# Performance work log

Hardware: AMD Instinct MI355X
Metric: run time of the kernel (lower is better)

Reference implementation:

```python
import jax, jax.numpy as jnp
import numpy as np

DIM = 1024
DIM_HEAD = 64
HEADS = 16
INNER = DIM_HEAD * HEADS
SCALE = 8.0
EPS_LN = 1e-5
EPS_L2 = 1e-12


def _layernorm(x, gamma):
    mu = jnp.mean(x, axis=-1, keepdims=True)
    var = jnp.var(x, axis=-1, keepdims=True)
    return (x - mu) / jnp.sqrt(var + EPS_LN) * gamma  # beta is a zero buffer


def _l2norm(t):
    n = jnp.linalg.norm(t, axis=-1, keepdims=True)
    return t / jnp.maximum(n, EPS_L2)


def setup_inputs() -> dict:
    key = jax.random.key(0)
    ks = jax.random.split(key, 8)
    b, n = 4, 2048
    x = jax.random.normal(ks[0], (b, n, DIM), dtype=jnp.float32)
    context_mask = jax.random.randint(ks[1], (b, n), 0, 2) > 0
    gamma = jnp.ones((DIM,), dtype=jnp.float32)
    wq = jax.random.normal(ks[2], (DIM, INNER), dtype=jnp.float32) * 0.02
    wkv = jax.random.normal(ks[3], (DIM, 2 * INNER), dtype=jnp.float32) * 0.02
    null_kv = jax.random.normal(ks[4], (2, HEADS, 1, DIM_HEAD), dtype=jnp.float32)
    q_scale = jnp.ones((DIM_HEAD,), dtype=jnp.float32)
    k_scale = jnp.ones((DIM_HEAD,), dtype=jnp.float32)
    wo = jax.random.normal(ks[5], (INNER, DIM), dtype=jnp.float32) * 0.02
    return {"x": x, "context_mask": context_mask, "gamma": gamma, "wq": wq,
            "wkv": wkv, "null_kv": null_kv, "q_scale": q_scale,
            "k_scale": k_scale, "wo": wo}


def reference(x, context_mask, gamma, wq, wkv, null_kv, q_scale, k_scale, wo):
    b, n, _ = x.shape
    xn = _layernorm(x, gamma)
    q = xn @ wq                     # [b, n, inner]
    kv = xn @ wkv                   # self-attention: kv_input = x
    k, v = jnp.split(kv, 2, axis=-1)

    def split_heads(t):
        return t.reshape(b, n, HEADS, DIM_HEAD).transpose(0, 2, 1, 3)  # b h n d

    q, k, v = map(split_heads, (q, k, v))
    nk = jnp.broadcast_to(null_kv[0][None], (b, HEADS, 1, DIM_HEAD))
    nv = jnp.broadcast_to(null_kv[1][None], (b, HEADS, 1, DIM_HEAD))
    k = jnp.concatenate([nk, k], axis=2)  # b h (n+1) d
    v = jnp.concatenate([nv, v], axis=2)

    q = _l2norm(q) * q_scale
    k = _l2norm(k) * k_scale

    sim = jnp.einsum('bhid,bhjd->bhij', q, k) * SCALE  # b h n (n+1)
    mask = jnp.pad(context_mask, ((0, 0), (1, 0)), constant_values=True)  # null kv always visible
    mask_value = -jnp.finfo(sim.dtype).max
    sim = jnp.where(mask[:, None, None, :], sim, mask_value)

    attn = jax.nn.softmax(sim, axis=-1)
    out = jnp.einsum('bhij,bhjd->bhid', attn, v)
    out = out.transpose(0, 2, 1, 3).reshape(b, n, INNER)
    return out @ wo
```

## Files before the change

kernel.cpp:

```cpp
#include <hip/hip_runtime.h>

typedef unsigned short u16;
typedef unsigned int u32;
typedef unsigned long long u64;
typedef __bf16 bf16x8 __attribute__((ext_vector_type(8)));
typedef float f32x4 __attribute__((ext_vector_type(4)));

#define B_ 4
#define N_ 2048
#define D_ 1024
#define H_ 16
#define DH_ 64
#define NKP_ 2112
#define NKT_ 33

__device__ __forceinline__ float bf2f(u16 u) {
  union { u32 i; float f; } v; v.i = ((u32)u) << 16; return v.f;
}
__device__ __forceinline__ u16 f2bf(float f) {
  union { float f; u32 i; } v; v.f = f;
  u32 r = v.i + 0x7fffu + ((v.i >> 16) & 1u);
  return (u16)(r >> 16);
}
__device__ __forceinline__ u32 cvtpk(float a, float b) {
  u32 r;
  asm("v_cvt_pk_bf16_f32 %0, %1, %2" : "=v"(r) : "v"(a), "v"(b));
  return r;
}
__device__ __forceinline__ void load_lds16(const void* g, void* l) {
  __builtin_amdgcn_global_load_lds((const __attribute__((address_space(1))) void*)g,
                                   (__attribute__((address_space(3))) void*)l, 16, 0, 0);
}

__global__ __launch_bounds__(256) void ln_kernel(const float* __restrict__ x,
                                                 const float* __restrict__ gamma,
                                                 u16* __restrict__ xn) {
  int row = blockIdx.x;
  int tid = threadIdx.x, lane = tid & 63, wid = tid >> 6;
  const float4 v = ((const float4*)(x + (size_t)row * D_))[tid];
  float s  = v.x + v.y + v.z + v.w;
  float ss = v.x * v.x + v.y * v.y + v.z * v.z + v.w * v.w;
#pragma unroll
  for (int off = 1; off < 64; off <<= 1) {
    s  += __shfl_xor(s,  off, 64);
    ss += __shfl_xor(ss, off, 64);
  }
  __shared__ float rs[4], rss[4];
  if (lane == 0) { rs[wid] = s; rss[wid] = ss; }
  __syncthreads();
  float S  = rs[0] + rs[1] + rs[2] + rs[3];
  float SS = rss[0] + rss[1] + rss[2] + rss[3];
  float mean = S * (1.0f / D_);
  float var  = SS * (1.0f / D_) - mean * mean;
  float inv  = rsqrtf(var + 1e-5f);
  const float4 g = ((const float4*)gamma)[tid];
  u16* o = xn + (size_t)row * D_ + tid * 4;
  o[0] = f2bf((v.x - mean) * inv * g.x);
  o[1] = f2bf((v.y - mean) * inv * g.y);
  o[2] = f2bf((v.z - mean) * inv * g.z);
  o[3] = f2bf((v.w - mean) * inv * g.w);
}

__global__ __launch_bounds__(256) void wt_kernel(const float* __restrict__ W,
                                                 u16* __restrict__ WT,
                                                 int K, int N) {
  __shared__ float t[32][33];
  int tiles_n = N >> 5;
  int tk = blockIdx.x / tiles_n, tn = blockIdx.x % tiles_n;
  int tx = threadIdx.x & 31, ty = threadIdx.x >> 5;
  int k0 = tk << 5, n0 = tn << 5;
#pragma unroll
  for (int i = 0; i < 4; ++i)
    t[ty + i * 8][tx] = W[(size_t)(k0 + ty + i * 8) * N + n0 + tx];
  __syncthreads();
#pragma unroll
  for (int i = 0; i < 4; ++i)
    WT[(size_t)(n0 + ty + i * 8) * K + k0 + tx] = f2bf(t[tx][ty + i * 8]);
}

__global__ __launch_bounds__(256) void prep_kernel(const int* __restrict__ mask,
                                                   const float* __restrict__ qs,
                                                   const float* __restrict__ ksc,
                                                   const float* __restrict__ null_kv,
                                                   u16* __restrict__ Kb,
                                                   u16* __restrict__ Vt,
                                                   float* __restrict__ cb) {
  __shared__ int cnts[4];
  int bh = blockIdx.x, h = bh & 15;
  int tid = threadIdx.x, lane = tid & 63, wid = tid >> 6;
  if (wid == 0) {
    float kv = null_kv[h * 64 + lane];
    float ss = kv * kv;
#pragma unroll
    for (int off = 1; off < 64; off <<= 1) ss += __shfl_xor(ss, off, 64);
    float inv = 1.0f / fmaxf(sqrtf(ss), 1e-12f);
    Kb[((size_t)bh * NKP_ + 2048) * 64 + lane] = f2bf(kv * inv * ksc[lane]);
    Vt[((size_t)bh * 64 + lane) * NKP_ + 2048] = f2bf(null_kv[1024 + h * 64 + lane]);
  }
  for (int i = tid; i < 63 * 64; i += 256) {
    int r = i >> 6, c = i & 63;
    Kb[((size_t)bh * NKP_ + 2049 + r) * 64 + c] = 0;
  }
  for (int i = tid; i < 64 * 63; i += 256) {
    int d = i / 63, c = i % 63;
    Vt[((size_t)bh * 64 + d) * NKP_ + 2049 + c] = 0;
  }
  if (bh == 0) {
    if (tid < 4) cnts[tid] = 0;
    __syncthreads();
    int c0 = 0, c1 = 0, c2 = 0, c3 = 0;
    for (int i = tid; i < B_ * N_; i += 256) {
      int z = (mask[i] == 0);
      int b = i >> 11;
      if (b == 0) c0 += z; else if (b == 1) c1 += z; else if (b == 2) c2 += z; else c3 += z;
    }
    atomicAdd(&cnts[0], c0); atomicAdd(&cnts[1], c1);
    atomicAdd(&cnts[2], c2); atomicAdd(&cnts[3], c3);
    __syncthreads();
    if (tid == 0) {
      float mw = 0.f;
      for (int i = 0; i < DH_; ++i) mw = fmaxf(mw, fabsf(qs[i] * ksc[i]));
      float cbias = -8.0f * mw * 1.4426950408889634f;
      cb[0] = cbias;
      float e = __builtin_amdgcn_exp2f(cbias);
#pragma unroll
      for (int b = 0; b < 4; ++b) cb[1 + b] = (float)(cnts[b] + 63) * e;
    }
  }
}

template <int MODE>
__global__ __launch_bounds__(256) void gemm_bt(const u16* __restrict__ A,
                                               const u16* __restrict__ Bt,
                                               void* __restrict__ Cv,
                                               int M, int N, int K,
                                               const float* __restrict__ qs,
                                               u16* __restrict__ Vt,
                                               const int* __restrict__ Mask) {
  __shared__ __attribute__((aligned(16))) u16 sm[2 * 128 * 64];
  u16* a_sm = sm;
  u16* b_sm = sm + 128 * 64;
  int tid = threadIdx.x, lane = tid & 63, wid = tid >> 6;
  int m0 = blockIdx.x * 128, n0 = blockIdx.y * 128;
  int wm = (wid >> 1) * 64, wn = (wid & 1) * 64;
  int sr = lane >> 3, sc = (lane & 7) * 8;
  int la = lane & 15, lk = (lane >> 4) * 8;
  f32x4 acc[4][4] = {};
  for (int k0 = 0; k0 < K; k0 += 64) {
    __syncthreads();
#pragma unroll
    for (int i = 0; i < 4; ++i) {
      int r = i * 32 + wid * 8;
      load_lds16(A  + (size_t)(m0 + r + sr) * K + k0 + sc, &a_sm[r * 64]);
      load_lds16(Bt + (size_t)(n0 + r + sr) * K + k0 + sc, &b_sm[r * 64]);
    }
    __syncthreads();
#pragma unroll
    for (int s = 0; s < 2; ++s) {
      bf16x8 af[4], bfr[4];
#pragma unroll
      for (int mf = 0; mf < 4; ++mf)
        af[mf] = *(const bf16x8*)&a_sm[(wm + mf * 16 + la) * 64 + s * 32 + lk];
#pragma unroll
      for (int nf = 0; nf < 4; ++nf)
        bfr[nf] = *(const bf16x8*)&b_sm[(wn + nf * 16 + la) * 64 + s * 32 + lk];
#pragma unroll
      for (int mf = 0; mf < 4; ++mf)
#pragma unroll
        for (int nf = 0; nf < 4; ++nf)
          acc[mf][nf] = __builtin_amdgcn_mfma_f32_16x16x32_bf16(af[mf], bfr[nf], acc[mf][nf], 0, 0, 0);
    }
  }
  int crow = (lane >> 4) * 4, ccol = lane & 15;

  if (MODE == 3) {
    int by = blockIdx.y;
    int rr0 = m0 + wm;
    int b = rr0 >> 11;
    int seq0 = rr0 & 2047;
    const int* mrow = Mask + b * N_ + seq0;
    if (by < 8) {
      int h = by * 2 + (wn >> 6);
      float kscv[4];
#pragma unroll
      for (int nf = 0; nf < 4; ++nf) kscv[nf] = qs[nf * 16 + ccol];
      u16* kb = (u16*)Cv + ((size_t)(b * 16 + h) * NKP_) * 64;
#pragma unroll
      for (int mf = 0; mf < 4; ++mf) {
        float invr[4]; int mvv[4];
#pragma unroll
        for (int r = 0; r < 4; ++r) {
          float ss = 0.f;
#pragma unroll
          for (int nf = 0; nf < 4; ++nf) ss += acc[mf][nf][r] * acc[mf][nf][r];
#pragma unroll
          for (int off = 1; off < 16; off <<= 1) ss += __shfl_xor(ss, off, 64);
          invr[r] = 1.0f / fmaxf(sqrtf(ss), 1e-12f);
          mvv[r] = mrow[mf * 16 + crow + r];
        }
#pragma unroll
        for (int nf = 0; nf < 4; ++nf)
#pragma unroll
          for (int r = 0; r < 4; ++r)
            kb[(size_t)(seq0 + mf * 16 + crow + r) * 64 + nf * 16 + ccol] =
                f2bf(mvv[r] ? acc[mf][nf][r] * invr[r] * kscv[nf] : 0.f);
      }
    } else {
      int h = (by - 8) * 2 + (wn >> 6);
      __syncthreads();
      u16* tw = sm + wid * 4096;
#pragma unroll
      for (int mf = 0; mf < 4; ++mf) {
        int mvv[4];
#pragma unroll
        for (int r = 0; r < 4; ++r) mvv[r] = mrow[mf * 16 + crow + r];
#pragma unroll
        for (int nf = 0; nf < 4; ++nf) {
          int row = nf * 16 + ccol;
#pragma unroll
          for (int r = 0; r < 4; ++r)
            tw[row * 64 + ((mf * 16 + crow + r) ^ ((row & 7) * 8))] =
                f2bf(mvv[r] ? acc[mf][nf][r] : 0.f);
        }
      }
      u16* vb = Vt + ((size_t)(b * 16 + h) * 64) * NKP_;
      int dr = lane >> 3, kc = (lane & 7) * 8;
#pragma unroll
      for (int i = 0; i < 8; ++i) {
        int d = i * 8 + dr;
        bf16x8 vv = *(const bf16x8*)&tw[d * 64 + (kc ^ ((d & 7) * 8))];
        *(bf16x8*)(vb + (size_t)d * NKP_ + seq0 + kc) = vv;
      }
    }
    return;
  }

  float qsv[4];
  if (MODE == 2) {
#pragma unroll
    for (int nf = 0; nf < 4; ++nf) qsv[nf] = qs[nf * 16 + ccol];
  }
#pragma unroll
  for (int mf = 0; mf < 4; ++mf) {
    float invr[4];
    if (MODE == 2) {
#pragma unroll
      for (int r = 0; r < 4; ++r) {
        float ss = 0.f;
#pragma unroll
        for (int nf = 0; nf < 4; ++nf) ss += acc[mf][nf][r] * acc[mf][nf][r];
#pragma unroll
        for (int off = 1; off < 16; off <<= 1) ss += __shfl_xor(ss, off, 64);
        invr[r] = 1.0f / fmaxf(sqrtf(ss), 1e-12f);
      }
    }
#pragma unroll
    for (int nf = 0; nf < 4; ++nf) {
      int rr = m0 + wm + mf * 16 + crow;
      int cc = n0 + wn + nf * 16 + ccol;
      if (MODE == 1) {
        float* C = (float*)Cv;
#pragma unroll
        for (int r = 0; r < 4; ++r) C[(size_t)(rr + r) * N + cc] = acc[mf][nf][r];
      } else if (MODE == 0) {
        u16* C = (u16*)Cv;
#pragma unroll
        for (int r = 0; r < 4; ++r) C[(size_t)(rr + r) * N + cc] = f2bf(acc[mf][nf][r]);
      } else {
        u16* C = (u16*)Cv;
#pragma unroll
        for (int r = 0; r < 4; ++r)
          C[(size_t)(rr + r) * N + cc] = f2bf(acc[mf][nf][r] * invr[r] * qsv[nf]);
      }
    }
  }
}

__global__ __launch_bounds__(512) void attn_kernel(const u16* __restrict__ Q,
                                                   const u16* __restrict__ Kb,
                                                   const u16* __restrict__ Vt,
                                                   const float* __restrict__ cb,
                                                   u16* __restrict__ O) {
  __shared__ __attribute__((aligned(16))) u16 k_sm[2][64 * 64];
  __shared__ __attribute__((aligned(16))) u16 v_sm[2][64 * 64];
  __shared__ __attribute__((aligned(16))) u16 p_sm[8][32 * 64];
  int tid = threadIdx.x, lane = tid & 63, wid = tid >> 6;
  int bh = blockIdx.x, b = bh >> 4, h = bh & 15;
  int q0 = blockIdx.y * 256 + wid * 32;
  int la = lane & 15, lk = (lane >> 4) * 8, crow = (lane >> 4) * 4;
  int swz = (la & 7) * 8;
  int sr = lane >> 3;
  int scz = ((lane & 7) ^ (lane >> 3)) * 8;

  bf16x8 aq[2][2];
#pragma unroll
  for (int qb = 0; qb < 2; ++qb) {
    const u16* qrow = Q + ((size_t)(b * N_) + q0 + qb * 16 + la) * D_ + h * DH_;
#pragma unroll
    for (int s = 0; s < 2; ++s) aq[qb][s] = *(const bf16x8*)(qrow + s * 32 + lk);
  }
  float l[2] = {0.f, 0.f};
  f32x4 o[2][4] = {};
  const u16* Kbh = Kb + (size_t)bh * NKP_ * 64;
  const u16* Vbh = Vt + (size_t)bh * 64 * NKP_;
  const float C1 = 11.541560327111707f;
  const float cbias = cb[0];
  const float lsub = cb[1 + b];

#define STAGE(bb, kt)                                                          \
  do {                                                                         \
    int key0_ = (kt) * 64;                                                     \
    int r_ = wid * 8;                                                          \
    load_lds16(Kbh + (size_t)(key0_ + r_ + sr) * 64 + scz, &k_sm[bb][r_ * 64]); \
    load_lds16(Vbh + (size_t)(r_ + sr) * NKP_ + key0_ + scz, &v_sm[bb][r_ * 64]); \
  } while (0)

  STAGE(0, 0);

#pragma unroll 2
  for (int kt = 0; kt < NKT_; ++kt) {
    int bb = kt & 1;
    __syncthreads();
    if (kt + 1 < NKT_) STAGE(bb ^ 1, kt + 1);

    f32x4 sacc[2][4] = {};
    __builtin_amdgcn_s_setprio(1);
#pragma unroll
    for (int nf = 0; nf < 4; ++nf) {
      bf16x8 bk0 = *(const bf16x8*)&k_sm[bb][(nf * 16 + la) * 64 + (lk ^ swz)];
      bf16x8 bk1 = *(const bf16x8*)&k_sm[bb][(nf * 16 + la) * 64 + ((32 + lk) ^ swz)];
#pragma unroll
      for (int qb = 0; qb < 2; ++qb) {
        sacc[qb][nf] = __builtin_amdgcn_mfma_f32_16x16x32_bf16(bk0, aq[qb][0], sacc[qb][nf], 0, 0, 0);
        sacc[qb][nf] = __builtin_amdgcn_mfma_f32_16x16x32_bf16(bk1, aq[qb][1], sacc[qb][nf], 0, 0, 0);
      }
    }
    __builtin_amdgcn_s_setprio(0);

#pragma unroll
    for (int nf = 0; nf < 4; ++nf) {
      int key = nf * 16 + crow;
#pragma unroll
      for (int qb = 0; qb < 2; ++qb) {
        float p0 = __builtin_amdgcn_exp2f(fmaf(sacc[qb][nf][0], C1, cbias));
        float p1 = __builtin_amdgcn_exp2f(fmaf(sacc[qb][nf][1], C1, cbias));
        float p2 = __builtin_amdgcn_exp2f(fmaf(sacc[qb][nf][2], C1, cbias));
        float p3 = __builtin_amdgcn_exp2f(fmaf(sacc[qb][nf][3], C1, cbias));
        l[qb] += (p0 + p1) + (p2 + p3);
        uint2 pw;
        pw.x = cvtpk(p0, p1);
        pw.y = cvtpk(p2, p3);
        *(uint2*)&p_sm[wid][(qb * 16 + la) * 64 + (key ^ swz)] = pw;
      }
    }

    __builtin_amdgcn_s_setprio(1);
#pragma unroll
    for (int s = 0; s < 2; ++s) {
      bf16x8 bv[4];
#pragma unroll
      for (int dt = 0; dt < 4; ++dt)
        bv[dt] = *(const bf16x8*)&v_sm[bb][(dt * 16 + la) * 64 + ((s * 32 + lk) ^ swz)];
#pragma unroll
      for (int qb = 0; qb < 2; ++qb) {
        bf16x8 ap = *(const bf16x8*)&p_sm[wid][(qb * 16 + la) * 64 + ((s * 32 + lk) ^ swz)];
#pragma unroll
        for (int dt = 0; dt < 4; ++dt)
          o[qb][dt] = __builtin_amdgcn_mfma_f32_16x16x32_bf16(ap, bv[dt], o[qb][dt], 0, 0, 0);
      }
    }
    __builtin_amdgcn_s_setprio(0);
  }
#undef STAGE

#pragma unroll
  for (int qb = 0; qb < 2; ++qb) {
    l[qb] += __shfl_xor(l[qb], 16, 64);
    l[qb] += __shfl_xor(l[qb], 32, 64);
#pragma unroll
    for (int r = 0; r < 4; ++r) {
      float lq = __shfl(l[qb], crow + r, 64) - lsub;
      float inv = 1.0f / lq;
      int n = q0 + qb * 16 + crow + r;
      u16* ob = O + ((size_t)(b * N_) + n) * D_ + h * DH_;
#pragma unroll
      for (int dt = 0; dt < 4; ++dt) ob[dt * 16 + la] = f2bf(o[qb][dt][r] * inv);
    }
  }
}

extern "C" void kernel_launch(void* const* d_in, const int* in_sizes, int n_in,
                              void* d_out, int out_size, void* d_ws, size_t ws_size,
                              hipStream_t stream) {
  (void)in_sizes; (void)n_in; (void)out_size; (void)ws_size;
  const float* x     = (const float*)d_in[0];
  const int*   mask  = (const int*)d_in[1];
  const float* gamma = (const float*)d_in[2];
  const float* wq    = (const float*)d_in[3];
  const float* wkv   = (const float*)d_in[4];
  const float* nkv   = (const float*)d_in[5];
  const float* qs    = (const float*)d_in[6];
  const float* ksc   = (const float*)d_in[7];
  const float* wo    = (const float*)d_in[8];

  char* ws   = (char*)d_ws;
  u16* xn    = (u16*)(ws);
  u16* wqT   = (u16*)(ws + (16ull << 20));
  u16* wkvT  = (u16*)(ws + (18ull << 20));
  u16* woT   = (u16*)(ws + (22ull << 20));
  u16* Kb    = (u16*)(ws + (24ull << 20));
  u16* Vt    = (u16*)(ws + (41ull << 20));
  float* cb  = (float*)(ws + (58ull << 20));
  u16* q_tmp = (u16*)d_out;
  u16* attn_out = xn;

  ln_kernel<<<B_ * N_, 256, 0, stream>>>(x, gamma, xn);
  wt_kernel<<<(1024 / 32) * (1024 / 32), 256, 0, stream>>>(wq, wqT, 1024, 1024);
  wt_kernel<<<(1024 / 32) * (2048 / 32), 256, 0, stream>>>(wkv, wkvT, 1024, 2048);
  wt_kernel<<<(1024 / 32) * (1024 / 32), 256, 0, stream>>>(wo, woT, 1024, 1024);
  prep_kernel<<<64, 256, 0, stream>>>(mask, qs, ksc, nkv, Kb, Vt, cb);
  gemm_bt<2><<<dim3(64, 8),  256, 0, stream>>>(xn, wqT,  q_tmp, 8192, 1024, 1024, qs, nullptr, nullptr);
  gemm_bt<3><<<dim3(64, 16), 256, 0, stream>>>(xn, wkvT, Kb,    8192, 2048, 1024, ksc, Vt, mask);
  attn_kernel<<<dim3(64, 8), 512, 0, stream>>>(q_tmp, Kb, Vt, cb, attn_out);
  gemm_bt<1><<<dim3(64, 8), 256, 0, stream>>>(attn_out, woT, (float*)d_out, 8192, 1024, 1024, nullptr, nullptr, nullptr);
}
```

Measured before the change: 231.7 us.

## Double-buffer GEMM LDS with swizzle and fuse Q/KV projections into one launch

The GEMM main loop now uses two LDS buffers, issuing the next K-tile load before computing the current one, so global loads overlap with MFMA work and one barrier per iteration is dropped. Both LDS tiles use an XOR swizzle to reduce bank conflicts on fragment reads. The Q and KV projection GEMMs are merged into one 24-column-block launch over a concatenated transposed weight. The layernorm output is written with one vector store per thread. The cost is double the shared memory per block, which may reduce occupancy, and K is now hardcoded to 1024.

```diff
diff --git a/kernel.cpp b/kernel.cpp
--- a/kernel.cpp
+++ b/kernel.cpp
@@ -54,11 +54,12 @@
   float var  = SS * (1.0f / D_) - mean * mean;
   float inv  = rsqrtf(var + 1e-5f);
   const float4 g = ((const float4*)gamma)[tid];
-  u16* o = xn + (size_t)row * D_ + tid * 4;
-  o[0] = f2bf((v.x - mean) * inv * g.x);
-  o[1] = f2bf((v.y - mean) * inv * g.y);
-  o[2] = f2bf((v.z - mean) * inv * g.z);
-  o[3] = f2bf((v.w - mean) * inv * g.w);
+  ushort4 o;
+  o.x = f2bf((v.x - mean) * inv * g.x);
+  o.y = f2bf((v.y - mean) * inv * g.y);
+  o.z = f2bf((v.z - mean) * inv * g.z);
+  o.w = f2bf((v.w - mean) * inv * g.w);
+  *(ushort4*)(xn + (size_t)row * D_ + tid * 4) = o;
 }
 
 __global__ __launch_bounds__(256) void wt_kernel(const float* __restrict__ W,
@@ -129,121 +130,70 @@
   }
 }
 
-template <int MODE>
-__global__ __launch_bounds__(256) void gemm_bt(const u16* __restrict__ A,
-                                               const u16* __restrict__ Bt,
-                                               void* __restrict__ Cv,
-                                               int M, int N, int K,
-                                               const float* __restrict__ qs,
-                                               u16* __restrict__ Vt,
-                                               const int* __restrict__ Mask) {
-  __shared__ __attribute__((aligned(16))) u16 sm[2 * 128 * 64];
-  u16* a_sm = sm;
-  u16* b_sm = sm + 128 * 64;
-  int tid = threadIdx.x, lane = tid & 63, wid = tid >> 6;
-  int m0 = blockIdx.x * 128, n0 = blockIdx.y * 128;
-  int wm = (wid >> 1) * 64, wn = (wid & 1) * 64;
-  int sr = lane >> 3, sc = (lane & 7) * 8;
-  int la = lane & 15, lk = (lane >> 4) * 8;
-  f32x4 acc[4][4] = {};
-  for (int k0 = 0; k0 < K; k0 += 64) {
-    __syncthreads();
-#pragma unroll
-    for (int i = 0; i < 4; ++i) {
-      int r = i * 32 + wid * 8;
-      load_lds16(A  + (size_t)(m0 + r + sr) * K + k0 + sc, &a_sm[r * 64]);
-      load_lds16(Bt + (size_t)(n0 + r + sr) * K + k0 + sc, &b_sm[r * 64]);
-    }
-    __syncthreads();
-#pragma unroll
-    for (int s = 0; s < 2; ++s) {
-      bf16x8 af[4], bfr[4];
-#pragma unroll
-      for (int mf = 0; mf < 4; ++mf)
-        af[mf] = *(const bf16x8*)&a_sm[(wm + mf * 16 + la) * 64 + s * 32 + lk];
-#pragma unroll
-      for (int nf = 0; nf < 4; ++nf)
-        bfr[nf] = *(const bf16x8*)&b_sm[(wn + nf * 16 + la) * 64 + s * 32 + lk];
-#pragma unroll
-      for (int mf = 0; mf < 4; ++mf)
-#pragma unroll
-        for (int nf = 0; nf < 4; ++nf)
-          acc[mf][nf] = __builtin_amdgcn_mfma_f32_16x16x32_bf16(af[mf], bfr[nf], acc[mf][nf], 0, 0, 0);
-    }
-  }
+#define GEMM_BODY(A, Bt)                                                       \
+  int tid = threadIdx.x, lane = tid & 63, wid = tid >> 6;                      \
+  int m0 = blockIdx.x * 128, n0 = blockIdx.y * 128;                            \
+  int wm = (wid >> 1) * 64, wn = (wid & 1) * 64;                               \
+  int sr = lane >> 3;                                                          \
+  int scz = ((lane & 7) ^ (lane >> 3)) * 8;       \
+  int la = lane & 15, lk = (lane >> 4) * 8;                                    \
+  int swz = (la & 7) * 8;                     \
+  f32x4 acc[4][4] = {};                                                        \
+  GSTAGE(0, 0);                                                                \
+  _Pragma("unroll 2")                                                          \
+  for (int kt = 0; kt < 16; ++kt) {                                            \
+    int bb = kt & 1;                                                           \
+    __syncthreads();                                                           \
+    if (kt + 1 < 16) GSTAGE(bb ^ 1, kt + 1);                                   \
+    _Pragma("unroll")                                                          \
+    for (int s = 0; s < 2; ++s) {                                              \
+      bf16x8 af[4], bfr[4];                                                    \
+      _Pragma("unroll")                                                        \
+      for (int mf = 0; mf < 4; ++mf)                                           \
+        af[mf] = *(const bf16x8*)&a_sm[bb][(wm + mf * 16 + la) * 64 + ((s * 32 + lk) ^ swz)]; \
+      _Pragma("unroll")                                                        \
+      for (int nf = 0; nf < 4; ++nf)                                           \
+        bfr[nf] = *(const bf16x8*)&b_sm[bb][(wn + nf * 16 + la) * 64 + ((s * 32 + lk) ^ swz)]; \
+      _Pragma("unroll")                                                        \
+      for (int mf = 0; mf < 4; ++mf)                                           \
+        _Pragma("unroll")                                                      \
+        for (int nf = 0; nf < 4; ++nf)                                         \
+          acc[mf][nf] = __builtin_amdgcn_mfma_f32_16x16x32_bf16(af[mf], bfr[nf], acc[mf][nf], 0, 0, 0); \
+    }                                                                          \
+  }                                                                            \
   int crow = (lane >> 4) * 4, ccol = lane & 15;
 
-  if (MODE == 3) {
-    int by = blockIdx.y;
-    int rr0 = m0 + wm;
-    int b = rr0 >> 11;
-    int seq0 = rr0 & 2047;
-    const int* mrow = Mask + b * N_ + seq0;
-    if (by < 8) {
-      int h = by * 2 + (wn >> 6);
-      float kscv[4];
-#pragma unroll
-      for (int nf = 0; nf < 4; ++nf) kscv[nf] = qs[nf * 16 + ccol];
-      u16* kb = (u16*)Cv + ((size_t)(b * 16 + h) * NKP_) * 64;
-#pragma unroll
-      for (int mf = 0; mf < 4; ++mf) {
-        float invr[4]; int mvv[4];
-#pragma unroll
-        for (int r = 0; r < 4; ++r) {
-          float ss = 0.f;
-#pragma unroll
-          for (int nf = 0; nf < 4; ++nf) ss += acc[mf][nf][r] * acc[mf][nf][r];
-#pragma unroll
-          for (int off = 1; off < 16; off <<= 1) ss += __shfl_xor(ss, off, 64);
-          invr[r] = 1.0f / fmaxf(sqrtf(ss), 1e-12f);
-          mvv[r] = mrow[mf * 16 + crow + r];
-        }
-#pragma unroll
-        for (int nf = 0; nf < 4; ++nf)
-#pragma unroll
-          for (int r = 0; r < 4; ++r)
-            kb[(size_t)(seq0 + mf * 16 + crow + r) * 64 + nf * 16 + ccol] =
-                f2bf(mvv[r] ? acc[mf][nf][r] * invr[r] * kscv[nf] : 0.f);
-      }
-    } else {
-      int h = (by - 8) * 2 + (wn >> 6);
-      __syncthreads();
-      u16* tw = sm + wid * 4096;
-#pragma unroll
-      for (int mf = 0; mf < 4; ++mf) {
-        int mvv[4];
-#pragma unroll
-        for (int r = 0; r < 4; ++r) mvv[r] = mrow[mf * 16 + crow + r];
-#pragma unroll
-        for (int nf = 0; nf < 4; ++nf) {
-          int row = nf * 16 + ccol;
-#pragma unroll
-          for (int r = 0; r < 4; ++r)
-            tw[row * 64 + ((mf * 16 + crow + r) ^ ((row & 7) * 8))] =
-                f2bf(mvv[r] ? acc[mf][nf][r] : 0.f);
-        }
-      }
-      u16* vb = Vt + ((size_t)(b * 16 + h) * 64) * NKP_;
-      int dr = lane >> 3, kc = (lane & 7) * 8;
-#pragma unroll
-      for (int i = 0; i < 8; ++i) {
-        int d = i * 8 + dr;
-        bf16x8 vv = *(const bf16x8*)&tw[d * 64 + (kc ^ ((d & 7) * 8))];
-        *(bf16x8*)(vb + (size_t)d * NKP_ + seq0 + kc) = vv;
-      }
-    }
-    return;
-  }
-
-  float qsv[4];
-  if (MODE == 2) {
+#define GSTAGE(bb, ks)                                                         \
+  do {                                                                         \
+    int k0_ = (ks) * 64;                                                       \
+    _Pragma("unroll")                                                          \
+    for (int i_ = 0; i_ < 4; ++i_) {                                           \
+      int r_ = wid * 32 + i_ * 8;                                              \
+      load_lds16(A + (size_t)(m0 + r_ + sr) * 1024 + k0_ + scz, &a_sm[bb][r_ * 64]); \
+      load_lds16(Bt + (size_t)(n0 + r_ + sr) * 1024 + k0_ + scz, &b_sm[bb][r_ * 64]); \
+    }                                                                          \
+  } while (0)
+
+__global__ __launch_bounds__(256) void gemm_qkv(const u16* __restrict__ A,
+                                                const u16* __restrict__ Bt,
+                                                u16* __restrict__ Qo,
+                                                u16* __restrict__ Kb,
+                                                u16* __restrict__ Vt,
+                                                const float* __restrict__ qs,
+                                                const float* __restrict__ ksc,
+                                                const int* __restrict__ Mask) {
+  __shared__ __attribute__((aligned(16))) u16 a_sm[2][128 * 64];
+  __shared__ __attribute__((aligned(16))) u16 b_sm[2][128 * 64];
+  GEMM_BODY(A, Bt)
+
+  int by = blockIdx.y;
+  if (by < 8) {
+    float qsv[4];
 #pragma unroll
     for (int nf = 0; nf < 4; ++nf) qsv[nf] = qs[nf * 16 + ccol];
-  }
-#pragma unroll
-  for (int mf = 0; mf < 4; ++mf) {
-    float invr[4];
-    if (MODE == 2) {
+#pragma unroll
+    for (int mf = 0; mf < 4; ++mf) {
+      float invr[4];
 #pragma unroll
       for (int r = 0; r < 4; ++r) {
         float ss = 0.f;
@@ -253,27 +203,92 @@
         for (int off = 1; off < 16; off <<= 1) ss += __shfl_xor(ss, off, 64);
         invr[r] = 1.0f / fmaxf(sqrtf(ss), 1e-12f);
       }
-    }
+#pragma unroll
+      for (int nf = 0; nf < 4; ++nf) {
+        int rr = m0 + wm + mf * 16 + crow;
+        int cc = n0 + wn + nf * 16 + ccol;
+#pragma unroll
+        for (int r = 0; r < 4; ++r)
+          Qo[(size_t)(rr + r) * 1024 + cc] = f2bf(acc[mf][nf][r] * invr[r] * qsv[nf]);
+      }
+    }
+    return;
+  }
+
+  int rr0 = m0 + wm;
+  int b = rr0 >> 11;
+  int seq0 = rr0 & 2047;
+  const int* mrow = Mask + b * N_ + seq0;
+  if (by < 16) {
+    int h = (by - 8) * 2 + (wn >> 6);
+    float kscv[4];
+#pragma unroll
+    for (int nf = 0; nf < 4; ++nf) kscv[nf] = ksc[nf * 16 + ccol];
+    u16* kb = Kb + ((size_t)(b * 16 + h) * NKP_) * 64;
+#pragma unroll
+    for (int mf = 0; mf < 4; ++mf) {
+      float invr[4]; int mvv[4];
+#pragma unroll
+      for (int r = 0; r < 4; ++r) {
+        float ss = 0.f;
+#pragma unroll
+        for (int nf = 0; nf < 4; ++nf) ss += acc[mf][nf][r] * acc[mf][nf][r];
+#pragma unroll
+        for (int off = 1; off < 16; off <<= 1) ss += __shfl_xor(ss, off, 64);
+        invr[r] = 1.0f / fmaxf(sqrtf(ss), 1e-12f);
+        mvv[r] = mrow[mf * 16 + crow + r];
+      }
+#pragma unroll
+      for (int nf = 0; nf < 4; ++nf)
+#pragma unroll
+        for (int r = 0; r < 4; ++r)
+          kb[(size_t)(seq0 + mf * 16 + crow + r) * 64 + nf * 16 + ccol] =
+              f2bf(mvv[r] ? acc[mf][nf][r] * invr[r] * kscv[nf] : 0.f);
+    }
+  } else {
+    int h = (by - 16) * 2 + (wn >> 6);
+    __syncthreads();
+    u16* tw = &a_sm[0][0] + wid * 4096;
+#pragma unroll
+    for (int mf = 0; mf < 4; ++mf) {
+      int mvv[4];
+#pragma unroll
+      for (int r = 0; r < 4; ++r) mvv[r] = mrow[mf * 16 + crow + r];
+#pragma unroll
+      for (int nf = 0; nf < 4; ++nf) {
+        int row = nf * 16 + ccol;
+#pragma unroll
+        for (int r = 0; r < 4; ++r)
+          tw[row * 64 + ((mf * 16 + crow + r) ^ ((row & 7) * 8))] =
+              f2bf(mvv[r] ? acc[mf][nf][r] : 0.f);
+      }
+    }
+    u16* vb = Vt + ((size_t)(b * 16 + h) * 64) * NKP_;
+    int dr = lane >> 3, kc = (lane & 7) * 8;
+#pragma unroll
+    for (int i = 0; i < 8; ++i) {
+      int d = i * 8 + dr;
+      bf16x8 vv = *(const bf16x8*)&tw[d * 64 + (kc ^ ((d & 7) * 8))];
+      *(bf16x8*)(vb + (size_t)d * NKP_ + seq0 + kc) = vv;
+    }
+  }
+}
+
+__global__ __launch_bounds__(256) void gemm_out(const u16* __restrict__ A,
+                                                const u16* __restrict__ Bt,
+                                                float* __restrict__ C) {
+  __shared__ __attribute__((aligned(16))) u16 a_sm[2][128 * 64];
+  __shared__ __attribute__((aligned(16))) u16 b_sm[2][128 * 64];
+  GEMM_BODY(A, Bt)
+#pragma unroll
+  for (int mf = 0; mf < 4; ++mf)
 #pragma unroll
     for (int nf = 0; nf < 4; ++nf) {
       int rr = m0 + wm + mf * 16 + crow;
       int cc = n0 + wn + nf * 16 + ccol;
-      if (MODE == 1) {
-        float* C = (float*)Cv;
-#pragma unroll
-        for (int r = 0; r < 4; ++r) C[(size_t)(rr + r) * N + cc] = acc[mf][nf][r];
-      } else if (MODE == 0) {
-        u16* C = (u16*)Cv;
-#pragma unroll
-        for (int r = 0; r < 4; ++r) C[(size_t)(rr + r) * N + cc] = f2bf(acc[mf][nf][r]);
-      } else {
-        u16* C = (u16*)Cv;
-#pragma unroll
-        for (int r = 0; r < 4; ++r)
-          C[(size_t)(rr + r) * N + cc] = f2bf(acc[mf][nf][r] * invr[r] * qsv[nf]);
-      }
-    }
-  }
+#pragma unroll
+      for (int r = 0; r < 4; ++r) C[(size_t)(rr + r) * 1024 + cc] = acc[mf][nf][r];
+    }
 }
 
 __global__ __launch_bounds__(512) void attn_kernel(const u16* __restrict__ Q,
@@ -405,8 +420,8 @@
 
   char* ws   = (char*)d_ws;
   u16* xn    = (u16*)(ws);
-  u16* wqT   = (u16*)(ws + (16ull << 20));
-  u16* wkvT  = (u16*)(ws + (18ull << 20));
+  u16* wqkvT = (u16*)(ws + (16ull << 20));
+  u16* wkvT  = wqkvT + 1024 * 1024;
   u16* woT   = (u16*)(ws + (22ull << 20));
   u16* Kb    = (u16*)(ws + (24ull << 20));
   u16* Vt    = (u16*)(ws + (41ull << 20));
@@ -415,12 +430,11 @@
   u16* attn_out = xn;
 
   ln_kernel<<<B_ * N_, 256, 0, stream>>>(x, gamma, xn);
-  wt_kernel<<<(1024 / 32) * (1024 / 32), 256, 0, stream>>>(wq, wqT, 1024, 1024);
+  wt_kernel<<<(1024 / 32) * (1024 / 32), 256, 0, stream>>>(wq, wqkvT, 1024, 1024);
   wt_kernel<<<(1024 / 32) * (2048 / 32), 256, 0, stream>>>(wkv, wkvT, 1024, 2048);
   wt_kernel<<<(1024 / 32) * (1024 / 32), 256, 0, stream>>>(wo, woT, 1024, 1024);
   prep_kernel<<<64, 256, 0, stream>>>(mask, qs, ksc, nkv, Kb, Vt, cb);
-  gemm_bt<2><<<dim3(64, 8),  256, 0, stream>>>(xn, wqT,  q_tmp, 8192, 1024, 1024, qs, nullptr, nullptr);
-  gemm_bt<3><<<dim3(64, 16), 256, 0, stream>>>(xn, wkvT, Kb,    8192, 2048, 1024, ksc, Vt, mask);
+  gemm_qkv<<<dim3(64, 24), 256, 0, stream>>>(xn, wqkvT, q_tmp, Kb, Vt, qs, ksc, mask);
   attn_kernel<<<dim3(64, 8), 512, 0, stream>>>(q_tmp, Kb, Vt, cb, attn_out);
-  gemm_bt<1><<<dim3(64, 8), 256, 0, stream>>>(attn_out, woT, (float*)d_out, 8192, 1024, 1024, nullptr, nullptr, nullptr);
-}
+  gemm_out<<<dim3(64, 8), 256, 0, stream>>>(attn_out, woT, (float*)d_out);
+}
```

Result: slower. 270.8 us (+16.9%).
